# Optimization experiments

Measured on AMD Instinct MI355X. Metric: run time of the kernel, lower is better.

Reference implementation:

```python
import jax, jax.numpy as jnp
import numpy as np

N = 100000   # nodes
E = 1600000  # edges (avg degree 16)
IN = 128     # in_channels
H = 128      # hidden_channels
OUT = 64     # out_channels
EPS = 1e-5   # BatchNorm eps


def setup_inputs() -> dict:
    key = jax.random.key(0)
    ks = jax.random.split(key, 12)
    s = lambda fan: 1.0 / np.sqrt(fan)
    return {
        "x": jax.random.normal(ks[0], (N, IN), dtype=jnp.float32),
        "edge_index": jax.random.randint(ks[1], (2, E), 0, N, dtype=jnp.int32),
        "edge_weight": jax.random.uniform(ks[2], (E,), dtype=jnp.float32),
        "W1": jax.random.normal(ks[3], (IN, H), dtype=jnp.float32) * s(IN),
        "b1": jnp.zeros((H,), dtype=jnp.float32),
        "gamma": jnp.ones((H,), dtype=jnp.float32),
        "beta": jnp.zeros((H,), dtype=jnp.float32),
        "W2": jax.random.normal(ks[4], (H, H), dtype=jnp.float32) * s(H),
        "b2": jnp.zeros((H,), dtype=jnp.float32),
        "Wf": jax.random.normal(ks[5], (H, OUT), dtype=jnp.float32) * s(H),
        "bf": jnp.zeros((OUT,), dtype=jnp.float32),
    }


def gcn_conv(x, W, b, src, dst, ew, n):
    """PyG GCNConv: symmetric-normalized aggregation with added self-loops."""
    xw = x @ W  # [N, H]
    # degree includes self-loop weight 1.0
    deg = jax.ops.segment_sum(ew, dst, num_segments=n) + 1.0
    dinv = jax.lax.rsqrt(deg)  # deg >= 1, no zero-division
    norm = dinv[src] * ew * dinv[dst]  # [E]
    agg = jax.ops.segment_sum(xw[src] * norm[:, None], dst, num_segments=n)
    agg = agg + xw * (dinv * dinv)[:, None]  # self-loop contribution
    return agg + b


def reference(x, edge_index, edge_weight, W1, b1, gamma, beta, W2, b2, Wf, bf):
    src, dst = edge_index[0], edge_index[1]
    n = x.shape[0]
    # layer 1: GCNConv -> BatchNorm (batch stats) -> ReLU (dropout = eval/identity)
    h = gcn_conv(x, W1, b1, src, dst, edge_weight, n)
    mu = h.mean(axis=0)
    var = ((h - mu) ** 2).mean(axis=0)
    h = gamma * (h - mu) * jax.lax.rsqrt(var + EPS) + beta
    h1 = jax.nn.relu(h)
    # layer 2: last GCNConv (no BN/ReLU)
    h2 = gcn_conv(h1, W2, b2, src, dst, edge_weight, n)
    # JumpingKnowledge 'max' over layer outputs, then final projection
    jk = jnp.maximum(h1, h2)
    return jk @ Wf + bf
```

## Files before the change

kernel.cpp:

```cpp
#include <hip/hip_runtime.h>

#define NN 100000
#define NE 1600000
#define EPSF 1e-5f

#define NB 1563
#define NCHUNK 256
#define CHUNK 6250
#define CAP 2048

typedef __attribute__((ext_vector_type(8))) short bf16x8;
typedef __attribute__((ext_vector_type(4))) float f32x4;

__device__ __forceinline__ ushort f2b(float f) {
    uint u = __float_as_uint(f);
    uint r = (u + 0x7FFFu + ((u >> 16) & 1u)) >> 16;
    return (ushort)r;
}
__device__ __forceinline__ float b2f(ushort h) { return __uint_as_float(((uint)h) << 16); }


__global__ __launch_bounds__(256) void hist_b(const int* __restrict__ ei, int* __restrict__ part) {
    __shared__ int h[NB];
    int chunk = blockIdx.x;
    for (int i = threadIdx.x; i < NB; i += 256) h[i] = 0;
    __syncthreads();
    int base = chunk * CHUNK;
    int lim = base + CHUNK; if (lim > NE) lim = NE;
    for (int e = base + threadIdx.x; e < lim; e += 256)
        atomicAdd(&h[ei[NE + e] >> 6], 1);
    __syncthreads();
    int* p = part + (size_t)chunk * NB;
    for (int i = threadIdx.x; i < NB; i += 256) p[i] = h[i];
}

__global__ __launch_bounds__(256) void scan_chunks_b(int* __restrict__ part, int* __restrict__ cnt) {
    int b = blockIdx.x * 256 + threadIdx.x;
    if (b >= NB) return;
    int acc = 0;
    for (int c = 0; c < NCHUNK; c++) {
        int v = part[(size_t)c * NB + b];
        part[(size_t)c * NB + b] = acc;
        acc += v;
    }
    cnt[b] = acc;
}

__global__ __launch_bounds__(256) void bucket_scan(const int* __restrict__ cnt, int* __restrict__ bstart) {
    __shared__ int s[256];
    int t = threadIdx.x;
    int loc[7];
    int sum = 0;
#pragma unroll
    for (int j = 0; j < 7; j++) {
        int i = t * 7 + j;
        int v = (i < NB) ? cnt[i] : 0;
        loc[j] = sum;
        sum += v;
    }
    s[t] = sum;
    __syncthreads();
    for (int off = 1; off < 256; off <<= 1) {
        int x = (t >= off) ? s[t - off] : 0;
        __syncthreads();
        s[t] += x;
        __syncthreads();
    }
    int base = t ? s[t - 1] : 0;
#pragma unroll
    for (int j = 0; j < 7; j++) {
        int i = t * 7 + j;
        if (i < NB) bstart[i] = base + loc[j];
    }
    if (t == 0) bstart[NB] = NE;
}

__global__ __launch_bounds__(256) void place_b(const int* __restrict__ ei, const float* __restrict__ ew,
                                               const int* __restrict__ bstart, const int* __restrict__ part,
                                               uint2* __restrict__ csr) {
    __shared__ int cur[NB];
    int chunk = blockIdx.x;
    const int* p = part + (size_t)chunk * NB;
    for (int i = threadIdx.x; i < NB; i += 256) cur[i] = bstart[i] + p[i];
    __syncthreads();
    int base = chunk * CHUNK;
    int lim = base + CHUNK; if (lim > NE) lim = NE;
    for (int e = base + threadIdx.x; e < lim; e += 256) {
        int s = ei[e], d = ei[NE + e];
        float w = ew[e];
        int pos = atomicAdd(&cur[d >> 6], 1);
        csr[pos] = make_uint2((uint)s | ((uint)(d & 63) << 17), __float_as_uint(w));
    }
}

__global__ __launch_bounds__(256) void subsort(uint2* __restrict__ csr, const int* __restrict__ bstart,
                                               int* __restrict__ row, float* __restrict__ dinv) {
    __shared__ uint2 E[CAP];
    __shared__ int cnt[64];
    __shared__ int cur[64];
    __shared__ float degf[64];
    int bkt = blockIdx.x;
    int beg = bstart[bkt], end = bstart[bkt + 1];
    int m = end - beg;
    if (threadIdx.x < 64) { cnt[threadIdx.x] = 0; degf[threadIdx.x] = 0.f; }
    __syncthreads();
    for (int i = threadIdx.x; i < m; i += 256) {
        uint2 ed = csr[beg + i];
        if (i < CAP) E[i] = ed;
        int dl = (ed.x >> 17) & 63;
        atomicAdd(&cnt[dl], 1);
        atomicAdd(&degf[dl], __uint_as_float(ed.y));
    }
    __syncthreads();
    if (threadIdx.x < 64) {
        int p = 0;
        for (int j = 0; j < (int)threadIdx.x; j++) p += cnt[j];
        cur[threadIdx.x] = p;
        int node = bkt * 64 + threadIdx.x;
        if (node < NN) {
            row[node] = beg + p;
            dinv[node] = rsqrtf(degf[threadIdx.x] + 1.0f);
        }
        if (bkt == NB - 1 && threadIdx.x == 0) row[NN] = NE;
    }
    __syncthreads();
    for (int i = threadIdx.x; i < m; i += 256) {
        uint2 ed = E[i < CAP ? i : 0];
        int dl = (ed.x >> 17) & 63;
        int pos = atomicAdd(&cur[dl], 1);
        csr[beg + pos] = make_uint2(ed.x & 0x1FFFFu, ed.y);
    }
}

__global__ __launch_bounds__(256) void norm_csr(uint2* __restrict__ csr, const int* __restrict__ row,
                                                const float* __restrict__ dinv, int n) {
    int wave = threadIdx.x >> 6, lane = threadIdx.x & 63;
    int node = blockIdx.x * 4 + wave;
    if (node >= n) return;
    int beg = row[node], end = row[node + 1];
    float di = dinv[node];
    for (int e = beg + lane; e < end; e += 64) {
        uint2 u = csr[e];
        csr[e].y = __float_as_uint(__uint_as_float(u.y) * dinv[u.x] * di);
    }
}


__global__ __launch_bounds__(256) void pack_w(const float* __restrict__ W, ushort* __restrict__ WF, int ncol) {
    int slot = blockIdx.x * 256 + threadIdx.x;
    int nc16 = ncol >> 4;
    int tot = 4 * nc16 * 64;
    if (slot >= tot) return;
    int lane = slot & 63;
    int c = (slot >> 6) % nc16;
    int ks = (slot >> 6) / nc16;
    int col = c * 16 + (lane & 15);
    int k0 = ks * 32 + (lane >> 4) * 8;
#pragma unroll
    for (int e = 0; e < 8; e++) WF[slot * 8 + e] = f2b(W[(k0 + e) * ncol + col]);
}


template <bool AF32>
__global__ __launch_bounds__(256) void gemm_mfma(const void* __restrict__ Ap, const ushort* __restrict__ WF,
                                                 ushort* __restrict__ C, int ngrp) {
    __shared__ ushort Bl[4 * 8 * 64 * 8];
    for (int i = threadIdx.x * 8; i < 4 * 8 * 64 * 8; i += 256 * 8)
        *(bf16x8*)&Bl[i] = *(const bf16x8*)&WF[i];
    __syncthreads();
    int wave = __builtin_amdgcn_readfirstlane(threadIdx.x >> 6);
    int lane = threadIdx.x & 63;
    int rg = blockIdx.x * 4 + wave;
    if (rg >= ngrp) return;
    int r0 = rg * 16;
    int rA = r0 + (lane & 15);
    int kb = (lane >> 4) * 8;
    bf16x8 a[4];
    if (AF32) {
        const float* A = (const float*)Ap;
#pragma unroll
        for (int ks = 0; ks < 4; ks++) {
            const float* p = &A[(size_t)rA * 128 + ks * 32 + kb];
            float4 x0 = *(const float4*)p;
            float4 x1 = *(const float4*)(p + 4);
            ushort t[8] = {f2b(x0.x), f2b(x0.y), f2b(x0.z), f2b(x0.w),
                           f2b(x1.x), f2b(x1.y), f2b(x1.z), f2b(x1.w)};
            a[ks] = *(bf16x8*)t;
        }
    } else {
        const ushort* A = (const ushort*)Ap;
#pragma unroll
        for (int ks = 0; ks < 4; ks++)
            a[ks] = *(const bf16x8*)&A[(size_t)rA * 128 + ks * 32 + kb];
    }
#pragma unroll
    for (int c = 0; c < 8; c++) {
        f32x4 acc = {0.f, 0.f, 0.f, 0.f};
#pragma unroll
        for (int ks = 0; ks < 4; ks++) {
            bf16x8 b = *(const bf16x8*)&Bl[((ks * 8 + c) * 64 + lane) * 8];
            acc = __builtin_amdgcn_mfma_f32_16x16x32_bf16(a[ks], b, acc, 0, 0, 0);
        }
        int colb = c * 16 + (lane & 15);
        int rowb = r0 + (lane >> 4) * 4;
#pragma unroll
        for (int r = 0; r < 4; r++)
            C[(size_t)(rowb + r) * 128 + colb] = f2b(acc[r]);
    }
}

__global__ __launch_bounds__(256) void gemm_mfma_bn(const ushort* __restrict__ HB, const float* __restrict__ stats,
                                                    const ushort* __restrict__ WF, ushort* __restrict__ H1,
                                                    ushort* __restrict__ C, int ngrp) {
    __shared__ ushort Bl[4 * 8 * 64 * 8];
    __shared__ float sst[256];
    sst[threadIdx.x] = stats[threadIdx.x];
    for (int i = threadIdx.x * 8; i < 4 * 8 * 64 * 8; i += 256 * 8)
        *(bf16x8*)&Bl[i] = *(const bf16x8*)&WF[i];
    __syncthreads();
    int wave = __builtin_amdgcn_readfirstlane(threadIdx.x >> 6);
    int lane = threadIdx.x & 63;
    int rg = blockIdx.x * 4 + wave;
    if (rg >= ngrp) return;
    int r0 = rg * 16;
    int rA = r0 + (lane & 15);
    int kb = (lane >> 4) * 8;
    bf16x8 a[4];
#pragma unroll
    for (int ks = 0; ks < 4; ks++) {
        int cbase = ks * 32 + kb;
        bf16x8 u = *(const bf16x8*)&HB[(size_t)rA * 128 + cbase];
        ushort t[8];
#pragma unroll
        for (int e = 0; e < 8; e++) {
            float f = fmaxf(b2f((ushort)u[e]) * sst[cbase + e] + sst[128 + cbase + e], 0.f);
            t[e] = f2b(f);
        }
        a[ks] = *(bf16x8*)t;
        *(bf16x8*)&H1[(size_t)rA * 128 + cbase] = a[ks];
    }
#pragma unroll
    for (int c = 0; c < 8; c++) {
        f32x4 acc = {0.f, 0.f, 0.f, 0.f};
#pragma unroll
        for (int ks = 0; ks < 4; ks++) {
            bf16x8 b = *(const bf16x8*)&Bl[((ks * 8 + c) * 64 + lane) * 8];
            acc = __builtin_amdgcn_mfma_f32_16x16x32_bf16(a[ks], b, acc, 0, 0, 0);
        }
        int colb = c * 16 + (lane & 15);
        int rowb = r0 + (lane >> 4) * 4;
#pragma unroll
        for (int r = 0; r < 4; r++)
            C[(size_t)(rowb + r) * 128 + colb] = f2b(acc[r]);
    }
}


__global__ __launch_bounds__(256) void final_mfma(const ushort* __restrict__ H1, const ushort* __restrict__ H2,
                                                  const ushort* __restrict__ WF, const float* __restrict__ bfv,
                                                  float* __restrict__ OUT, int ngrp) {
    __shared__ ushort Bl[4 * 4 * 64 * 8];
    for (int i = threadIdx.x * 8; i < 4 * 4 * 64 * 8; i += 256 * 8)
        *(bf16x8*)&Bl[i] = *(const bf16x8*)&WF[i];
    __syncthreads();
    int wave = __builtin_amdgcn_readfirstlane(threadIdx.x >> 6);
    int lane = threadIdx.x & 63;
    int rg = blockIdx.x * 4 + wave;
    if (rg >= ngrp) return;
    int r0 = rg * 16;
    int rA = r0 + (lane & 15);
    int kb = (lane >> 4) * 8;
    bf16x8 a[4];
#pragma unroll
    for (int ks = 0; ks < 4; ks++) {
        bf16x8 u = *(const bf16x8*)&H1[(size_t)rA * 128 + ks * 32 + kb];
        bf16x8 v = *(const bf16x8*)&H2[(size_t)rA * 128 + ks * 32 + kb];
        ushort t[8];
#pragma unroll
        for (int e = 0; e < 8; e++) {
            ushort ue = (ushort)u[e], ve = (ushort)v[e];
            t[e] = (b2f(ue) >= b2f(ve)) ? ue : ve;
        }
        a[ks] = *(bf16x8*)t;
    }
#pragma unroll
    for (int c = 0; c < 4; c++) {
        f32x4 acc = {0.f, 0.f, 0.f, 0.f};
#pragma unroll
        for (int ks = 0; ks < 4; ks++) {
            bf16x8 b = *(const bf16x8*)&Bl[((ks * 4 + c) * 64 + lane) * 8];
            acc = __builtin_amdgcn_mfma_f32_16x16x32_bf16(a[ks], b, acc, 0, 0, 0);
        }
        int colb = c * 16 + (lane & 15);
        int rowb = r0 + (lane >> 4) * 4;
        float bb = bfv[colb];
#pragma unroll
        for (int r = 0; r < 4; r++)
            OUT[(size_t)(rowb + r) * 64 + colb] = acc[r] + bb;
    }
}


__global__ __launch_bounds__(256) void aggregate_b2(const ushort* __restrict__ XW, const int* __restrict__ row,
                                                    const uint2* __restrict__ csr, const float* __restrict__ dinv,
                                                    const float* __restrict__ bias, ushort* __restrict__ OUT, int n) {
    int wave = __builtin_amdgcn_readfirstlane(threadIdx.x >> 6);
    int lane = threadIdx.x & 63;
    int node = blockIdx.x * 4 + wave;
    if (node >= n) return;
    int beg = row[node], end = row[node + 1];
    float ax = 0.f, ay = 0.f;
    int e = beg;
    for (; e + 3 < end; e += 4) {
        uint2 p0 = csr[e], p1 = csr[e + 1], p2 = csr[e + 2], p3 = csr[e + 3];
        uint v0 = *(const uint*)&XW[(size_t)p0.x * 128 + lane * 2];
        uint v1 = *(const uint*)&XW[(size_t)p1.x * 128 + lane * 2];
        uint v2 = *(const uint*)&XW[(size_t)p2.x * 128 + lane * 2];
        uint v3 = *(const uint*)&XW[(size_t)p3.x * 128 + lane * 2];
        float w0 = __uint_as_float(p0.y), w1 = __uint_as_float(p1.y);
        float w2 = __uint_as_float(p2.y), w3 = __uint_as_float(p3.y);
        ax += w0 * __uint_as_float(v0 << 16) + w1 * __uint_as_float(v1 << 16) +
              w2 * __uint_as_float(v2 << 16) + w3 * __uint_as_float(v3 << 16);
        ay += w0 * __uint_as_float(v0 & 0xFFFF0000u) + w1 * __uint_as_float(v1 & 0xFFFF0000u) +
              w2 * __uint_as_float(v2 & 0xFFFF0000u) + w3 * __uint_as_float(v3 & 0xFFFF0000u);
    }
    for (; e < end; e++) {
        uint2 p0 = csr[e];
        float w0 = __uint_as_float(p0.y);
        uint v0 = *(const uint*)&XW[(size_t)p0.x * 128 + lane * 2];
        ax += w0 * __uint_as_float(v0 << 16);
        ay += w0 * __uint_as_float(v0 & 0xFFFF0000u);
    }
    float di = dinv[node], sl = di * di;
    uint vs = *(const uint*)&XW[(size_t)node * 128 + lane * 2];
    float ox = ax + sl * __uint_as_float(vs << 16) + bias[lane * 2];
    float oy = ay + sl * __uint_as_float(vs & 0xFFFF0000u) + bias[lane * 2 + 1];
    uint o = (uint)f2b(ox) | ((uint)f2b(oy) << 16);
    *(uint*)&OUT[(size_t)node * 128 + lane * 2] = o;
}


__global__ __launch_bounds__(256) void bn_stats_b(const ushort* __restrict__ H, float* __restrict__ part, int n) {
    int wave = threadIdx.x >> 6;
    int lane = threadIdx.x & 63;
    float2 s = make_float2(0.f, 0.f), q = make_float2(0.f, 0.f);
    for (int r = blockIdx.x * 4 + wave; r < n; r += gridDim.x * 4) {
        uint v = *(const uint*)&H[(size_t)r * 128 + lane * 2];
        float x = __uint_as_float(v << 16);
        float y = __uint_as_float(v & 0xFFFF0000u);
        s.x += x; s.y += y;
        q.x += x * x; q.y += y * y;
    }
    __shared__ float2 reds[4][64];
    __shared__ float2 redq[4][64];
    reds[wave][lane] = s;
    redq[wave][lane] = q;
    __syncthreads();
    if (threadIdx.x < 64) {
        int l = threadIdx.x;
        float2 S = make_float2(0.f, 0.f), Q = make_float2(0.f, 0.f);
#pragma unroll
        for (int w = 0; w < 4; w++) {
            S.x += reds[w][l].x; S.y += reds[w][l].y;
            Q.x += redq[w][l].x; Q.y += redq[w][l].y;
        }
        part[blockIdx.x * 256 + l * 2 + 0] = S.x;
        part[blockIdx.x * 256 + l * 2 + 1] = S.y;
        part[blockIdx.x * 256 + 128 + l * 2 + 0] = Q.x;
        part[blockIdx.x * 256 + 128 + l * 2 + 1] = Q.y;
    }
}

__global__ __launch_bounds__(1024) void bn_final2(const float* __restrict__ part, const float* __restrict__ gamma,
                                                  const float* __restrict__ beta, float* __restrict__ stats,
                                                  float invN) {
    int c = threadIdx.x & 127;
    int g = threadIdx.x >> 7;
    float s = 0.f, q = 0.f;
#pragma unroll 8
    for (int b = g; b < 512; b += 8) {
        s += part[b * 256 + c];
        q += part[b * 256 + 128 + c];
    }
    __shared__ float red[8][256];
    red[g][c] = s;
    red[g][128 + c] = q;
    __syncthreads();
    __shared__ float fin[256];
    if (threadIdx.x < 256) {
        float acc = 0.f;
#pragma unroll
        for (int gg = 0; gg < 8; gg++) acc += red[gg][threadIdx.x];
        fin[threadIdx.x] = acc;
    }
    __syncthreads();
    if (threadIdx.x < 128) {
        float mu = fin[c] * invN;
        float var = fin[128 + c] * invN - mu * mu;
        float sc = gamma[c] * rsqrtf(var + EPSF);
        stats[c] = sc;
        stats[128 + c] = beta[c] - mu * sc;
    }
}


extern "C" void kernel_launch(void* const* d_in, const int* in_sizes, int n_in,
                              void* d_out, int out_size, void* d_ws, size_t ws_size,
                              hipStream_t stream) {
    const float* x     = (const float*)d_in[0];
    const int*   ei    = (const int*)  d_in[1];
    const float* ew    = (const float*)d_in[2];
    const float* W1    = (const float*)d_in[3];
    const float* b1    = (const float*)d_in[4];
    const float* gamma = (const float*)d_in[5];
    const float* beta  = (const float*)d_in[6];
    const float* W2    = (const float*)d_in[7];
    const float* b2    = (const float*)d_in[8];
    const float* Wf    = (const float*)d_in[9];
    const float* bf    = (const float*)d_in[10];
    float* out = (float*)d_out;

    char* ws = (char*)d_ws;
    size_t off = 0;
    auto alloc = [&](size_t bytes) {
        void* p = ws + off;
        off += (bytes + 1023) & ~(size_t)1023;
        return p;
    };
    ushort* XWB  = (ushort*)alloc((size_t)NN * 128 * 2);
    ushort* HB   = (ushort*)alloc((size_t)NN * 128 * 2);
    ushort* H1B  = (ushort*)alloc((size_t)NN * 128 * 2);
    ushort* H2B  = (ushort*)alloc((size_t)NN * 128 * 2);
    float*  DINV = (float*) alloc((size_t)NN * 4);
    int*    ROW  = (int*)   alloc((size_t)(NN + 1) * 4);
    int*    CNT  = (int*)   alloc((size_t)NB * 4);
    int*    BSTART = (int*) alloc((size_t)(NB + 1) * 4);
    uint2*  CSR8 = (uint2*) alloc((size_t)NE * 8);
    float*  PARTBN = (float*)alloc((size_t)512 * 256 * 4);
    float*  STAT = (float*) alloc(1024);
    ushort* WF1  = (ushort*)alloc((size_t)4 * 8 * 64 * 8 * 2);
    ushort* WF2  = (ushort*)alloc((size_t)4 * 8 * 64 * 8 * 2);
    ushort* WFF  = (ushort*)alloc((size_t)4 * 4 * 64 * 8 * 2);
    int* PART = (int*)XWB;

    int ngrp = NN / 16;
    int gblocks = (ngrp + 3) / 4;

    hist_b<<<NCHUNK, 256, 0, stream>>>(ei, PART);
    scan_chunks_b<<<(NB + 255) / 256, 256, 0, stream>>>(PART, CNT);
    bucket_scan<<<1, 256, 0, stream>>>(CNT, BSTART);
    place_b<<<NCHUNK, 256, 0, stream>>>(ei, ew, BSTART, PART, CSR8);
    subsort<<<NB, 256, 0, stream>>>(CSR8, BSTART, ROW, DINV);
    norm_csr<<<(NN + 3) / 4, 256, 0, stream>>>(CSR8, ROW, DINV, NN);

    pack_w<<<8, 256, 0, stream>>>(W1, WF1, 128);
    pack_w<<<8, 256, 0, stream>>>(W2, WF2, 128);
    pack_w<<<4, 256, 0, stream>>>(Wf, WFF, 64);

    gemm_mfma<true><<<gblocks, 256, 0, stream>>>(x, WF1, XWB, ngrp);
    aggregate_b2<<<(NN + 3) / 4, 256, 0, stream>>>(XWB, ROW, CSR8, DINV, b1, HB, NN);
    bn_stats_b<<<512, 256, 0, stream>>>(HB, PARTBN, NN);
    bn_final2<<<1, 1024, 0, stream>>>(PARTBN, gamma, beta, STAT, 1.0f / NN);

    gemm_mfma_bn<<<gblocks, 256, 0, stream>>>(HB, STAT, WF2, H1B, XWB, ngrp);
    aggregate_b2<<<(NN + 3) / 4, 256, 0, stream>>>(XWB, ROW, CSR8, DINV, b2, H2B, NN);

    final_mfma<<<gblocks, 256, 0, stream>>>(H1B, H2B, WFF, bf, out, ngrp);
}
```

Before: 288.9 us.

## Channel-block XW layout with packed 4-byte CSR edges for cache-local aggregation

The GEMMs now write XW in a channel-blocked layout ([8 blocks][N][16]), so each aggregation block gathers only a 3.2 MB slice that can stay resident in cache. Each of the 8 block groups handles 16 nodes for one channel slice. Edges are packed into 4 bytes (17-bit source index plus an fp16 normalized weight), which halves CSR traffic, and the CSR is now read 8 times instead of once. Each node's edge list is split across 4 lane groups and reduced with shuffles. The fp16 weights lose precision, and lanes that cover only 32 bytes per gather may reduce coalescing efficiency.

```diff
diff --git a/kernel.cpp b/kernel.cpp
--- a/kernel.cpp
+++ b/kernel.cpp
@@ -1,4 +1,5 @@
 #include <hip/hip_runtime.h>
+#include <hip/hip_fp16.h>
 
 #define NN 100000
 #define NE 1600000
@@ -132,8 +133,8 @@
     }
 }
 
-__global__ __launch_bounds__(256) void norm_csr(uint2* __restrict__ csr, const int* __restrict__ row,
-                                                const float* __restrict__ dinv, int n) {
+__global__ __launch_bounds__(256) void norm4(const uint2* __restrict__ csr, const int* __restrict__ row,
+                                             const float* __restrict__ dinv, uint* __restrict__ csr4, int n) {
     int wave = threadIdx.x >> 6, lane = threadIdx.x & 63;
     int node = blockIdx.x * 4 + wave;
     if (node >= n) return;
@@ -141,7 +142,9 @@
     float di = dinv[node];
     for (int e = beg + lane; e < end; e += 64) {
         uint2 u = csr[e];
-        csr[e].y = __float_as_uint(__uint_as_float(u.y) * dinv[u.x] * di);
+        float w = __uint_as_float(u.y) * dinv[u.x & 0x1FFFFu] * di;
+        ushort hb = __half_as_ushort(__float2half(w));
+        csr4[e] = (u.x & 0x1FFFFu) | ((uint)hb << 17);
     }
 }
 
@@ -163,7 +166,7 @@
 
 template <bool AF32>
 __global__ __launch_bounds__(256) void gemm_mfma(const void* __restrict__ Ap, const ushort* __restrict__ WF,
-                                                 ushort* __restrict__ C, int ngrp) {
+                                                 ushort* __restrict__ XWT, int ngrp) {
     __shared__ ushort Bl[4 * 8 * 64 * 8];
     for (int i = threadIdx.x * 8; i < 4 * 8 * 64 * 8; i += 256 * 8)
         *(bf16x8*)&Bl[i] = *(const bf16x8*)&WF[i];
@@ -201,17 +204,17 @@
             bf16x8 b = *(const bf16x8*)&Bl[((ks * 8 + c) * 64 + lane) * 8];
             acc = __builtin_amdgcn_mfma_f32_16x16x32_bf16(a[ks], b, acc, 0, 0, 0);
         }
-        int colb = c * 16 + (lane & 15);
+        int chl = lane & 15;
         int rowb = r0 + (lane >> 4) * 4;
 #pragma unroll
         for (int r = 0; r < 4; r++)
-            C[(size_t)(rowb + r) * 128 + colb] = f2b(acc[r]);
+            XWT[((size_t)c * NN + rowb + r) * 16 + chl] = f2b(acc[r]);
     }
 }
 
 __global__ __launch_bounds__(256) void gemm_mfma_bn(const ushort* __restrict__ HB, const float* __restrict__ stats,
                                                     const ushort* __restrict__ WF, ushort* __restrict__ H1,
-                                                    ushort* __restrict__ C, int ngrp) {
+                                                    ushort* __restrict__ XWT, int ngrp) {
     __shared__ ushort Bl[4 * 8 * 64 * 8];
     __shared__ float sst[256];
     sst[threadIdx.x] = stats[threadIdx.x];
@@ -247,11 +250,11 @@
             bf16x8 b = *(const bf16x8*)&Bl[((ks * 8 + c) * 64 + lane) * 8];
             acc = __builtin_amdgcn_mfma_f32_16x16x32_bf16(a[ks], b, acc, 0, 0, 0);
         }
-        int colb = c * 16 + (lane & 15);
+        int chl = lane & 15;
         int rowb = r0 + (lane >> 4) * 4;
 #pragma unroll
         for (int r = 0; r < 4; r++)
-            C[(size_t)(rowb + r) * 128 + colb] = f2b(acc[r]);
+            XWT[((size_t)c * NN + rowb + r) * 16 + chl] = f2b(acc[r]);
     }
 }
 
@@ -301,42 +304,42 @@
 }
 
 
-__global__ __launch_bounds__(256) void aggregate_b2(const ushort* __restrict__ XW, const int* __restrict__ row,
-                                                    const uint2* __restrict__ csr, const float* __restrict__ dinv,
-                                                    const float* __restrict__ bias, ushort* __restrict__ OUT, int n) {
-    int wave = __builtin_amdgcn_readfirstlane(threadIdx.x >> 6);
+__global__ __launch_bounds__(512) void aggregate_c(const ushort* __restrict__ XWT, const int* __restrict__ row,
+                                                   const uint* __restrict__ csr4, const float* __restrict__ dinv,
+                                                   const float* __restrict__ bias, ushort* __restrict__ OUT) {
+    int cb = blockIdx.x & 7;
+    int nb = blockIdx.x >> 3;
+    int wv = threadIdx.x >> 6;
     int lane = threadIdx.x & 63;
-    int node = blockIdx.x * 4 + wave;
-    if (node >= n) return;
-    int beg = row[node], end = row[node + 1];
+    int half = lane >> 5;
+    int sub = lane & 31;
+    int eg = sub >> 3;
+    int cp = sub & 7;
+    int node = nb * 16 + wv * 2 + half;
+    int beg = __builtin_nontemporal_load(&row[node]);
+    int end = __builtin_nontemporal_load(&row[node + 1]);
+    const ushort* base = XWT + (size_t)cb * NN * 16;
     float ax = 0.f, ay = 0.f;
-    int e = beg;
-    for (; e + 3 < end; e += 4) {
-        uint2 p0 = csr[e], p1 = csr[e + 1], p2 = csr[e + 2], p3 = csr[e + 3];
-        uint v0 = *(const uint*)&XW[(size_t)p0.x * 128 + lane * 2];
-        uint v1 = *(const uint*)&XW[(size_t)p1.x * 128 + lane * 2];
-        uint v2 = *(const uint*)&XW[(size_t)p2.x * 128 + lane * 2];
-        uint v3 = *(const uint*)&XW[(size_t)p3.x * 128 + lane * 2];
-        float w0 = __uint_as_float(p0.y), w1 = __uint_as_float(p1.y);
-        float w2 = __uint_as_float(p2.y), w3 = __uint_as_float(p3.y);
-        ax += w0 * __uint_as_float(v0 << 16) + w1 * __uint_as_float(v1 << 16) +
-              w2 * __uint_as_float(v2 << 16) + w3 * __uint_as_float(v3 << 16);
-        ay += w0 * __uint_as_float(v0 & 0xFFFF0000u) + w1 * __uint_as_float(v1 & 0xFFFF0000u) +
-              w2 * __uint_as_float(v2 & 0xFFFF0000u) + w3 * __uint_as_float(v3 & 0xFFFF0000u);
-    }
-    for (; e < end; e++) {
-        uint2 p0 = csr[e];
-        float w0 = __uint_as_float(p0.y);
-        uint v0 = *(const uint*)&XW[(size_t)p0.x * 128 + lane * 2];
-        ax += w0 * __uint_as_float(v0 << 16);
-        ay += w0 * __uint_as_float(v0 & 0xFFFF0000u);
-    }
-    float di = dinv[node], sl = di * di;
-    uint vs = *(const uint*)&XW[(size_t)node * 128 + lane * 2];
-    float ox = ax + sl * __uint_as_float(vs << 16) + bias[lane * 2];
-    float oy = ay + sl * __uint_as_float(vs & 0xFFFF0000u) + bias[lane * 2 + 1];
-    uint o = (uint)f2b(ox) | ((uint)f2b(oy) << 16);
-    *(uint*)&OUT[(size_t)node * 128 + lane * 2] = o;
+    for (int i = beg + eg; i < end; i += 4) {
+        uint ed = __builtin_nontemporal_load(&csr4[i]);
+        int src = ed & 0x1FFFFu;
+        float w = __half2float(__ushort_as_half((ushort)(ed >> 17)));
+        uint v = *(const uint*)&base[(size_t)src * 16 + cp * 2];
+        ax += w * __uint_as_float(v << 16);
+        ay += w * __uint_as_float(v & 0xFFFF0000u);
+    }
+    ax += __shfl_xor(ax, 8);  ay += __shfl_xor(ay, 8);
+    ax += __shfl_xor(ax, 16); ay += __shfl_xor(ay, 16);
+    if (eg == 0) {
+        float di = __builtin_nontemporal_load(&dinv[node]);
+        float sl = di * di;
+        uint vs = *(const uint*)&base[(size_t)node * 16 + cp * 2];
+        float2 b = *(const float2*)&bias[cb * 16 + cp * 2];
+        float ox = ax + sl * __uint_as_float(vs << 16) + b.x;
+        float oy = ay + sl * __uint_as_float(vs & 0xFFFF0000u) + b.y;
+        uint o = (uint)f2b(ox) | ((uint)f2b(oy) << 16);
+        __builtin_nontemporal_store(o, (uint*)&OUT[(size_t)node * 128 + cb * 16 + cp * 2]);
+    }
 }
 
 
@@ -427,7 +430,7 @@
         off += (bytes + 1023) & ~(size_t)1023;
         return p;
     };
-    ushort* XWB  = (ushort*)alloc((size_t)NN * 128 * 2);
+    ushort* XWT  = (ushort*)alloc((size_t)NN * 128 * 2);
     ushort* HB   = (ushort*)alloc((size_t)NN * 128 * 2);
     ushort* H1B  = (ushort*)alloc((size_t)NN * 128 * 2);
     ushort* H2B  = (ushort*)alloc((size_t)NN * 128 * 2);
@@ -436,34 +439,36 @@
     int*    CNT  = (int*)   alloc((size_t)NB * 4);
     int*    BSTART = (int*) alloc((size_t)(NB + 1) * 4);
     uint2*  CSR8 = (uint2*) alloc((size_t)NE * 8);
+    uint*   CSR4 = (uint*)  alloc((size_t)NE * 4);
     float*  PARTBN = (float*)alloc((size_t)512 * 256 * 4);
     float*  STAT = (float*) alloc(1024);
     ushort* WF1  = (ushort*)alloc((size_t)4 * 8 * 64 * 8 * 2);
     ushort* WF2  = (ushort*)alloc((size_t)4 * 8 * 64 * 8 * 2);
     ushort* WFF  = (ushort*)alloc((size_t)4 * 4 * 64 * 8 * 2);
-    int* PART = (int*)XWB;
+    int* PART = (int*)XWT;
 
     int ngrp = NN / 16;
     int gblocks = (ngrp + 3) / 4;
+    int ablocks = (NN / 16) * 8;
 
     hist_b<<<NCHUNK, 256, 0, stream>>>(ei, PART);
     scan_chunks_b<<<(NB + 255) / 256, 256, 0, stream>>>(PART, CNT);
     bucket_scan<<<1, 256, 0, stream>>>(CNT, BSTART);
     place_b<<<NCHUNK, 256, 0, stream>>>(ei, ew, BSTART, PART, CSR8);
     subsort<<<NB, 256, 0, stream>>>(CSR8, BSTART, ROW, DINV);
-    norm_csr<<<(NN + 3) / 4, 256, 0, stream>>>(CSR8, ROW, DINV, NN);
+    norm4<<<(NN + 3) / 4, 256, 0, stream>>>(CSR8, ROW, DINV, CSR4, NN);
 
     pack_w<<<8, 256, 0, stream>>>(W1, WF1, 128);
     pack_w<<<8, 256, 0, stream>>>(W2, WF2, 128);
     pack_w<<<4, 256, 0, stream>>>(Wf, WFF, 64);
 
-    gemm_mfma<true><<<gblocks, 256, 0, stream>>>(x, WF1, XWB, ngrp);
-    aggregate_b2<<<(NN + 3) / 4, 256, 0, stream>>>(XWB, ROW, CSR8, DINV, b1, HB, NN);
+    gemm_mfma<true><<<gblocks, 256, 0, stream>>>(x, WF1, XWT, ngrp);
+    aggregate_c<<<ablocks, 512, 0, stream>>>(XWT, ROW, CSR4, DINV, b1, HB);
     bn_stats_b<<<512, 256, 0, stream>>>(HB, PARTBN, NN);
     bn_final2<<<1, 1024, 0, stream>>>(PARTBN, gamma, beta, STAT, 1.0f / NN);
 
-    gemm_mfma_bn<<<gblocks, 256, 0, stream>>>(HB, STAT, WF2, H1B, XWB, ngrp);
-    aggregate_b2<<<(NN + 3) / 4, 256, 0, stream>>>(XWB, ROW, CSR8, DINV, b2, H2B, NN);
+    gemm_mfma_bn<<<gblocks, 256, 0, stream>>>(HB, STAT, WF2, H1B, XWT, ngrp);
+    aggregate_c<<<ablocks, 512, 0, stream>>>(XWT, ROW, CSR4, DINV, b2, H2B);
 
     final_mfma<<<gblocks, 256, 0, stream>>>(H1B, H2B, WFF, bf, out, ngrp);
 }
```

Result: slower. 678.2 us (+134.8%).

## Pack CSR edges into 4-byte words with fp16 weights and unroll aggregation by eight

Applied to the files above, without the earlier changes.

The normalization pass now writes a compact 4-byte CSR entry that holds a 17-bit source index plus a 15-bit truncated fp16 edge weight (the sign bit is dropped), replacing the 8-byte index/float pair. The aggregation kernel reads these entries with nontemporal loads and unrolls by eight with two accumulator pairs to keep more gathers in flight. This halves the edge-stream traffic in both aggregation passes at the cost of reduced weight precision, which relies on the normalized weights being non-negative.

```diff
diff --git a/kernel.cpp b/kernel.cpp
--- a/kernel.cpp
+++ b/kernel.cpp
@@ -1,4 +1,5 @@
 #include <hip/hip_runtime.h>
+#include <hip/hip_fp16.h>
 
 #define NN 100000
 #define NE 1600000
@@ -132,8 +133,8 @@
     }
 }
 
-__global__ __launch_bounds__(256) void norm_csr(uint2* __restrict__ csr, const int* __restrict__ row,
-                                                const float* __restrict__ dinv, int n) {
+__global__ __launch_bounds__(256) void norm4(const uint2* __restrict__ csr, const int* __restrict__ row,
+                                             const float* __restrict__ dinv, uint* __restrict__ csr4, int n) {
     int wave = threadIdx.x >> 6, lane = threadIdx.x & 63;
     int node = blockIdx.x * 4 + wave;
     if (node >= n) return;
@@ -141,7 +142,9 @@
     float di = dinv[node];
     for (int e = beg + lane; e < end; e += 64) {
         uint2 u = csr[e];
-        csr[e].y = __float_as_uint(__uint_as_float(u.y) * dinv[u.x] * di);
+        float w = __uint_as_float(u.y) * dinv[u.x & 0x1FFFFu] * di;
+        ushort hb = __half_as_ushort(__float2half(w));
+        csr4[e] = (u.x & 0x1FFFFu) | ((uint)hb << 17);
     }
 }
 
@@ -301,36 +304,58 @@
 }
 
 
-__global__ __launch_bounds__(256) void aggregate_b2(const ushort* __restrict__ XW, const int* __restrict__ row,
-                                                    const uint2* __restrict__ csr, const float* __restrict__ dinv,
+__global__ __launch_bounds__(256) void aggregate_b4(const ushort* __restrict__ XW, const int* __restrict__ row,
+                                                    const uint* __restrict__ csr4, const float* __restrict__ dinv,
                                                     const float* __restrict__ bias, ushort* __restrict__ OUT, int n) {
     int wave = __builtin_amdgcn_readfirstlane(threadIdx.x >> 6);
     int lane = threadIdx.x & 63;
     int node = blockIdx.x * 4 + wave;
     if (node >= n) return;
     int beg = row[node], end = row[node + 1];
-    float ax = 0.f, ay = 0.f;
+    float ax0 = 0.f, ay0 = 0.f, ax1 = 0.f, ay1 = 0.f;
     int e = beg;
-    for (; e + 3 < end; e += 4) {
-        uint2 p0 = csr[e], p1 = csr[e + 1], p2 = csr[e + 2], p3 = csr[e + 3];
-        uint v0 = *(const uint*)&XW[(size_t)p0.x * 128 + lane * 2];
-        uint v1 = *(const uint*)&XW[(size_t)p1.x * 128 + lane * 2];
-        uint v2 = *(const uint*)&XW[(size_t)p2.x * 128 + lane * 2];
-        uint v3 = *(const uint*)&XW[(size_t)p3.x * 128 + lane * 2];
-        float w0 = __uint_as_float(p0.y), w1 = __uint_as_float(p1.y);
-        float w2 = __uint_as_float(p2.y), w3 = __uint_as_float(p3.y);
-        ax += w0 * __uint_as_float(v0 << 16) + w1 * __uint_as_float(v1 << 16) +
-              w2 * __uint_as_float(v2 << 16) + w3 * __uint_as_float(v3 << 16);
-        ay += w0 * __uint_as_float(v0 & 0xFFFF0000u) + w1 * __uint_as_float(v1 & 0xFFFF0000u) +
-              w2 * __uint_as_float(v2 & 0xFFFF0000u) + w3 * __uint_as_float(v3 & 0xFFFF0000u);
+    for (; e + 7 < end; e += 8) {
+        uint q0 = __builtin_nontemporal_load(&csr4[e + 0]);
+        uint q1 = __builtin_nontemporal_load(&csr4[e + 1]);
+        uint q2 = __builtin_nontemporal_load(&csr4[e + 2]);
+        uint q3 = __builtin_nontemporal_load(&csr4[e + 3]);
+        uint q4 = __builtin_nontemporal_load(&csr4[e + 4]);
+        uint q5 = __builtin_nontemporal_load(&csr4[e + 5]);
+        uint q6 = __builtin_nontemporal_load(&csr4[e + 6]);
+        uint q7 = __builtin_nontemporal_load(&csr4[e + 7]);
+        uint v0 = *(const uint*)&XW[(size_t)(q0 & 0x1FFFFu) * 128 + lane * 2];
+        uint v1 = *(const uint*)&XW[(size_t)(q1 & 0x1FFFFu) * 128 + lane * 2];
+        uint v2 = *(const uint*)&XW[(size_t)(q2 & 0x1FFFFu) * 128 + lane * 2];
+        uint v3 = *(const uint*)&XW[(size_t)(q3 & 0x1FFFFu) * 128 + lane * 2];
+        uint v4 = *(const uint*)&XW[(size_t)(q4 & 0x1FFFFu) * 128 + lane * 2];
+        uint v5 = *(const uint*)&XW[(size_t)(q5 & 0x1FFFFu) * 128 + lane * 2];
+        uint v6 = *(const uint*)&XW[(size_t)(q6 & 0x1FFFFu) * 128 + lane * 2];
+        uint v7 = *(const uint*)&XW[(size_t)(q7 & 0x1FFFFu) * 128 + lane * 2];
+        float w0 = __half2float(__ushort_as_half((ushort)(q0 >> 17)));
+        float w1 = __half2float(__ushort_as_half((ushort)(q1 >> 17)));
+        float w2 = __half2float(__ushort_as_half((ushort)(q2 >> 17)));
+        float w3 = __half2float(__ushort_as_half((ushort)(q3 >> 17)));
+        float w4 = __half2float(__ushort_as_half((ushort)(q4 >> 17)));
+        float w5 = __half2float(__ushort_as_half((ushort)(q5 >> 17)));
+        float w6 = __half2float(__ushort_as_half((ushort)(q6 >> 17)));
+        float w7 = __half2float(__ushort_as_half((ushort)(q7 >> 17)));
+        ax0 += w0 * __uint_as_float(v0 << 16) + w1 * __uint_as_float(v1 << 16) +
+               w2 * __uint_as_float(v2 << 16) + w3 * __uint_as_float(v3 << 16);
+        ay0 += w0 * __uint_as_float(v0 & 0xFFFF0000u) + w1 * __uint_as_float(v1 & 0xFFFF0000u) +
+               w2 * __uint_as_float(v2 & 0xFFFF0000u) + w3 * __uint_as_float(v3 & 0xFFFF0000u);
+        ax1 += w4 * __uint_as_float(v4 << 16) + w5 * __uint_as_float(v5 << 16) +
+               w6 * __uint_as_float(v6 << 16) + w7 * __uint_as_float(v7 << 16);
+        ay1 += w4 * __uint_as_float(v4 & 0xFFFF0000u) + w5 * __uint_as_float(v5 & 0xFFFF0000u) +
+               w6 * __uint_as_float(v6 & 0xFFFF0000u) + w7 * __uint_as_float(v7 & 0xFFFF0000u);
     }
     for (; e < end; e++) {
-        uint2 p0 = csr[e];
-        float w0 = __uint_as_float(p0.y);
-        uint v0 = *(const uint*)&XW[(size_t)p0.x * 128 + lane * 2];
-        ax += w0 * __uint_as_float(v0 << 16);
-        ay += w0 * __uint_as_float(v0 & 0xFFFF0000u);
-    }
+        uint q0 = __builtin_nontemporal_load(&csr4[e]);
+        uint v0 = *(const uint*)&XW[(size_t)(q0 & 0x1FFFFu) * 128 + lane * 2];
+        float w0 = __half2float(__ushort_as_half((ushort)(q0 >> 17)));
+        ax0 += w0 * __uint_as_float(v0 << 16);
+        ay0 += w0 * __uint_as_float(v0 & 0xFFFF0000u);
+    }
+    float ax = ax0 + ax1, ay = ay0 + ay1;
     float di = dinv[node], sl = di * di;
     uint vs = *(const uint*)&XW[(size_t)node * 128 + lane * 2];
     float ox = ax + sl * __uint_as_float(vs << 16) + bias[lane * 2];
@@ -436,6 +461,7 @@
     int*    CNT  = (int*)   alloc((size_t)NB * 4);
     int*    BSTART = (int*) alloc((size_t)(NB + 1) * 4);
     uint2*  CSR8 = (uint2*) alloc((size_t)NE * 8);
+    uint*   CSR4 = (uint*)  alloc((size_t)NE * 4);
     float*  PARTBN = (float*)alloc((size_t)512 * 256 * 4);
     float*  STAT = (float*) alloc(1024);
     ushort* WF1  = (ushort*)alloc((size_t)4 * 8 * 64 * 8 * 2);
@@ -451,19 +477,19 @@
     bucket_scan<<<1, 256, 0, stream>>>(CNT, BSTART);
     place_b<<<NCHUNK, 256, 0, stream>>>(ei, ew, BSTART, PART, CSR8);
     subsort<<<NB, 256, 0, stream>>>(CSR8, BSTART, ROW, DINV);
-    norm_csr<<<(NN + 3) / 4, 256, 0, stream>>>(CSR8, ROW, DINV, NN);
+    norm4<<<(NN + 3) / 4, 256, 0, stream>>>(CSR8, ROW, DINV, CSR4, NN);
 
     pack_w<<<8, 256, 0, stream>>>(W1, WF1, 128);
     pack_w<<<8, 256, 0, stream>>>(W2, WF2, 128);
     pack_w<<<4, 256, 0, stream>>>(Wf, WFF, 64);
 
     gemm_mfma<true><<<gblocks, 256, 0, stream>>>(x, WF1, XWB, ngrp);
-    aggregate_b2<<<(NN + 3) / 4, 256, 0, stream>>>(XWB, ROW, CSR8, DINV, b1, HB, NN);
+    aggregate_b4<<<(NN + 3) / 4, 256, 0, stream>>>(XWB, ROW, CSR4, DINV, b1, HB, NN);
     bn_stats_b<<<512, 256, 0, stream>>>(HB, PARTBN, NN);
     bn_final2<<<1, 1024, 0, stream>>>(PARTBN, gamma, beta, STAT, 1.0f / NN);
 
     gemm_mfma_bn<<<gblocks, 256, 0, stream>>>(HB, STAT, WF2, H1B, XWB, ngrp);
-    aggregate_b2<<<(NN + 3) / 4, 256, 0, stream>>>(XWB, ROW, CSR8, DINV, b2, H2B, NN);
+    aggregate_b4<<<(NN + 3) / 4, 256, 0, stream>>>(XWB, ROW, CSR4, DINV, b2, H2B, NN);
 
     final_mfma<<<gblocks, 256, 0, stream>>>(H1B, H2B, WFF, bf, out, ngrp);
 }
```

After: 283.5 us. About the same (-1.8%).
